# Kernel optimization log

Hardware: AMD Instinct MI355X
Metric: run time of the kernel (lower is better)

## Reference

```python
import jax, jax.numpy as jnp
import numpy as np

EPS = 1e-6
DIM_HEAD = 32
INP = 128
OUP = 128
IH = IW = 32


def _conv3x3(x, w):
    # NCHW conv, 3x3, stride 1, pad 1, no bias
    return jax.lax.conv_general_dilated(
        x, w, window_strides=(1, 1), padding=((1, 1), (1, 1)),
        dimension_numbers=("NCHW", "OIHW", "NCHW"))


def _groupnorm1(x, gamma, beta):
    # GroupNorm with 1 group: normalize over (C,H,W) per sample
    m = jnp.mean(x, axis=(1, 2, 3), keepdims=True)
    v = jnp.var(x, axis=(1, 2, 3), keepdims=True)
    xn = (x - m) * jax.lax.rsqrt(v + EPS)
    return xn * gamma[None, :, None, None] + beta[None, :, None, None]


def _proj(x, w, gamma, beta):
    return jax.nn.gelu(_groupnorm1(_conv3x3(x, w), gamma, beta), approximate=False)


def _relative_index(ih, iw):
    coords = np.stack(np.meshgrid(np.arange(ih), np.arange(iw), indexing="ij"))
    coords = coords.reshape(2, -1)  # (2, N)
    rel = coords[:, :, None] - coords[:, None, :]  # (2, N, N)
    rel[0] += ih - 1
    rel[1] += iw - 1
    rel[0] *= 2 * iw - 1
    return rel.sum(0).reshape(-1).astype(np.int32)  # (N*N,)


def setup_inputs() -> dict:
    key = jax.random.key(0)
    ks = jax.random.split(key, 12)
    B = 16
    x = jax.random.normal(ks[0], (B, INP, IH, IW), jnp.float32)
    w_scale = 0.05
    wq = jax.random.normal(ks[1], (INP, INP, 3, 3), jnp.float32) * w_scale
    wk = jax.random.normal(ks[2], (INP, INP, 3, 3), jnp.float32) * w_scale
    wv = jax.random.normal(ks[3], (INP, INP, 3, 3), jnp.float32) * w_scale
    gq = jnp.ones((INP,), jnp.float32); bq = jnp.zeros((INP,), jnp.float32)
    gk = jnp.ones((INP,), jnp.float32); bk = jnp.zeros((INP,), jnp.float32)
    gv = jnp.ones((INP,), jnp.float32); bv = jnp.zeros((INP,), jnp.float32)
    heads = INP // DIM_HEAD
    table = jax.random.normal(ks[4], ((2 * IH - 1) * (2 * IW - 1), heads), jnp.float32) * 0.02
    rel_index = jnp.asarray(_relative_index(IH, IW))
    out_w = jax.random.normal(ks[5], (OUP, INP, 1, 1), jnp.float32) * w_scale
    out_b = jnp.zeros((OUP,), jnp.float32)
    return {"x": x, "wq": wq, "gq": gq, "bq": bq, "wk": wk, "gk": gk, "bk": bk,
            "wv": wv, "gv": gv, "bv": bv, "table": table, "rel_index": rel_index,
            "out_w": out_w, "out_b": out_b}


def reference(x, wq, gq, bq, wk, gk, bk, wv, gv, bv, table, rel_index, out_w, out_b):
    B, C, ih, iw = x.shape
    H = C // DIM_HEAD
    N = ih * iw

    def to_heads(t):
        # b c ih iw -> b (ihiw) c -> b h n d (heads-major channel split)
        return t.reshape(B, C, N).transpose(0, 2, 1).reshape(B, N, H, DIM_HEAD).transpose(0, 2, 1, 3)

    q = to_heads(_proj(x, wq, gq, bq))
    k = to_heads(_proj(x, wk, gk, bk))
    v = to_heads(_proj(x, wv, gv, bv))

    # NOTE: original applies self.scale only when y is not None; y=None here -> no scale
    dots = jnp.einsum("bhnd,bhmd->bhnm", q, k)  # (B,H,N,N)

    bias = table[rel_index]                 # (N*N, H)
    bias = bias.reshape(N, N, H).transpose(2, 0, 1)[None]  # (1,H,N,N)
    attn = jax.nn.softmax(dots + bias, axis=-1)

    out = jnp.einsum("bhnm,bhmd->bhnd", attn, v)
    out = out.transpose(0, 2, 1, 3).reshape(B, N, C).transpose(0, 2, 1).reshape(B, C, ih, iw)
    # to_out: 1x1 conv + bias (Dropout2d is identity in eval)
    out = jax.lax.conv_general_dilated(
        out, out_w, window_strides=(1, 1), padding=((0, 0), (0, 0)),
        dimension_numbers=("NCHW", "OIHW", "NCHW")) + out_b[None, :, None, None]
    return out
```

## Files before the change

kernel.cpp:

```cpp
#include <hip/hip_runtime.h>

typedef unsigned short u16;
typedef unsigned int   u32;

#define NB   16
#define NC   128
#define NPIX 1024
#define NH   4
#define DH   32

typedef __attribute__((ext_vector_type(8))) short short8;
typedef __attribute__((ext_vector_type(4))) float f32x4;
typedef __attribute__((ext_vector_type(8))) _Float16 half8;

#define XROWS 1152

__device__ __forceinline__ float bf2f(u16 u) {
    return __uint_as_float(((u32)u) << 16);
}
__device__ __forceinline__ u16 f2bf(float f) {
    u32 u = __float_as_uint(f);
    u32 r = (u + 0x7fffu + ((u >> 16) & 1u)) >> 16;
    return (u16)r;
}
__device__ __forceinline__ u16 f2h(float f) {
    _Float16 h = (_Float16)f;
    u16 r; __builtin_memcpy(&r, &h, 2); return r;
}
__device__ __forceinline__ float h2f(u16 u) {
    _Float16 h; __builtin_memcpy(&h, &u, 2); return (float)h;
}
__device__ __forceinline__ int pk_h2(float a, float b) {
    auto h = __builtin_amdgcn_cvt_pkrtz(a, b);
    int r; __builtin_memcpy(&r, &h, 4); return r;
}
__device__ __forceinline__ float loadf(const void* p, int i, int isf) {
    return isf ? ((const float*)p)[i] : bf2f(((const u16*)p)[i]);
}
__device__ __forceinline__ float4 load4(const void* p, int i4, int isf) {
    if (isf) return ((const float4*)p)[i4];
    ushort4 u = ((const ushort4*)p)[i4];
    return make_float4(bf2f(u.x), bf2f(u.y), bf2f(u.z), bf2f(u.w));
}
__device__ __forceinline__ int detect_isf(const void* x) {
    const u16* p = (const u16*)x;
    u16 v = p[threadIdx.x & 63];
    int e = (v >> 7) & 0xFF;
    unsigned long long m = __ballot(e >= 134);
    return m != 0ull ? 1 : 0;
}

__global__ __launch_bounds__(256) void prep_all(
        const void* __restrict__ x,
        const void* __restrict__ w0, const void* __restrict__ w1,
        const void* __restrict__ w2, const void* __restrict__ ow,
        const int* __restrict__ rel, const void* __restrict__ table,
        u16* __restrict__ Wt, u16* __restrict__ Wf, u16* __restrict__ xTp,
        u16* __restrict__ biasT, float* __restrict__ stats) {
    __shared__ __align__(16) u32 smem_u[4160];
    int isf = detect_isf(x);
    int bid = blockIdx.x;
    int t = threadIdx.x;

    if (bid < 1792) {
        if (bid == 0 && t < 96) stats[t] = 0.f;
        int i = bid * 256 + t;
        if (i < 442368) {
            int j   = i / 147456;
            int rr  = i % 147456;
            int tap = rr >> 14;
            int co  = (rr >> 7) & 127;
            int ci  = rr & 127;
            const void* w = (j == 0) ? w0 : ((j == 1) ? w1 : w2);
            float v = loadf(w, (co * 128 + ci) * 9 + tap, isf);
            int coh = (co >> 6) & 1, wm = (co >> 5) & 1;
            int mt  = (co >> 4) & 1, l16 = co & 15;
            int ks  = (ci >> 5) & 3, q  = (ci >> 3) & 3, e = ci & 7;
            int dst = (j * 9 + tap) * 16384
                    + (coh * 2 + wm) * 4096 + ks * 1024 + mt * 512
                    + (q * 16 + l16) * 8 + e;
            Wt[dst] = f2bf(v);
        } else {
            int i2 = i - 442368;
            if (i2 < 16384) {
                int co = i2 >> 7, k = i2 & 127;
                int zc = (co >> 6) & 1, wm = (co >> 5) & 1;
                int mt = (co >> 4) & 1, l16 = co & 15;
                int ks = (k >> 5) & 3, q = (k >> 3) & 3, e = k & 7;
                int dst = (zc * 2 + wm) * 4096 + ks * 1024 + mt * 512
                        + (q * 16 + l16) * 8 + e;
                Wf[dst] = f2h(loadf(ow, i2, isf));
            }
        }
    } else if (bid < 2304) {
        float* tile = (float*)smem_u;
        int b2 = bid - 1792;
        int pixg = b2 & 7, cig = (b2 >> 3) & 3, b = b2 >> 5;

        if (pixg == 0 || pixg == 7) {
            int row = (pixg == 0 ? 0 : 1088) + (t >> 2);
            int seg = t & 3;
            size_t dst = ((size_t)(b * XROWS + row)) * 128 + cig * 32 + seg * 8;
            *(uint4*)&xTp[dst] = make_uint4(0, 0, 0, 0);
        }

        int ci = t >> 3, px0 = (t & 7) * 16;
        int base = b * (NC * NPIX) + (cig * 32 + ci) * NPIX + pixg * 128 + px0;
#pragma unroll
        for (int u = 0; u < 4; ++u) {
            float4 v = load4(x, (base >> 2) + u, isf);
            float* d = &tile[ci * 129 + px0 + u * 4];
            d[0] = v.x; d[1] = v.y; d[2] = v.z; d[3] = v.w;
        }
        __syncthreads();
#pragma unroll
        for (int u = 0; u < 2; ++u) {
            int c = t + u * 256;
            int pix = c >> 2, seg = c & 3;
            u16 tmp[8];
#pragma unroll
            for (int e = 0; e < 8; ++e)
                tmp[e] = f2bf(tile[(seg * 8 + e) * 129 + pix]);
            size_t dst = ((size_t)(b * XROWS + 64 + pixg * 128 + pix)) * 128
                       + cig * 32 + seg * 8;
            *(ushort4*)&xTp[dst] =
                make_ushort4(tmp[0], tmp[1], tmp[2], tmp[3]);
            *(ushort4*)&xTp[dst + 4] =
                make_ushort4(tmp[4], tmp[5], tmp[6], tmp[7]);
        }
    } else {
        int* rl = (int*)smem_u;
        int b2 = bid - 2304;
        int nt = b2 & 15, mt = b2 >> 4;

#pragma unroll
        for (int c = 0; c < 16; ++c) {
            int i = t + c * 256;
            int r = i >> 6, cc = i & 63;
            rl[r * 65 + cc] = rel[(size_t)(nt * 64 + r) * 1024 + mt * 64 + cc];
        }
        __syncthreads();

#pragma unroll
        for (int h = 0; h < NH; ++h) {
#pragma unroll
            for (int c = 0; c < 16; ++c) {
                int wdx = t + c * 256;
                int r     = wdx & 3;
                int lane  = (wdx >> 2) & 63;
                int fragl = wdx >> 8;
                int n16l  = fragl >> 2;
                int m16l  = fragl & 3;
                int n_loc = n16l * 16 + (lane & 15);
                int m_loc = m16l * 16 + ((lane >> 4) << 2) + r;
                int ri = rl[n_loc * 65 + m_loc];
                float v = loadf(table, ri * NH + h, isf);
                biasT[((size_t)h << 20)
                      + ((size_t)((nt * 4 + n16l) * 64 + (mt * 4 + m16l)) << 8)
                      + lane * 4 + r] = f2bf(v);
            }
        }
    }
}

__global__ __launch_bounds__(256) void conv6_kernel(
        const u16* __restrict__ xTp, const u16* __restrict__ Wt,
        u16* __restrict__ conv_out, float* __restrict__ stats) {
    __shared__ __align__(16) u16 Xh[194 * 128];

    int t = threadIdx.x;
    int bx = blockIdx.x, b = blockIdx.y, j = blockIdx.z;
    int pt = bx >> 1, coh = bx & 1;
    int p0 = pt * 128;
    int w = t >> 6, lane = t & 63;
    int q = lane >> 4, l16 = lane & 15;
    int cobase = coh * 64 + (w & 1) * 32;
    int pixbase = (w >> 1) * 64;

    const u16* xb  = xTp + ((size_t)b * XROWS + 64) * 128;
    const u16* wrb = Wt + (size_t)(j * 9) * 16384
                   + (coh * 2 + (w & 1)) * 4096 + lane * 8;

    short8 awA[2][4], awB[2][4];
#pragma unroll
    for (int ks = 0; ks < 4; ++ks) {
        awA[0][ks] = *(const short8*)(wrb + ks * 1024);
        awA[1][ks] = *(const short8*)(wrb + ks * 1024 + 512);
    }

#pragma unroll
    for (int k = 0; k < 13; ++k) {
        int c = t + k * 256;
        if (c < 194 * 16) {
            int row = c >> 4, seg = c & 15;
            int pg = p0 - 33 + row;
            uint4 v = *(const uint4*)(xb + (size_t)pg * 128 + seg * 8);
            *(uint4*)&Xh[row * 128 + ((seg + row) & 15) * 8] = v;
        }
    }
    __syncthreads();

    f32x4 acc[2][4];
#pragma unroll
    for (int mt = 0; mt < 2; ++mt)
#pragma unroll
        for (int nt = 0; nt < 4; ++nt) acc[mt][nt] = (f32x4)0.f;

#pragma unroll
    for (int tap = 0; tap < 9; ++tap) {
        const int dy = tap / 3, dx = tap % 3;
        bool inv_e = (dx == 0) && (l16 == 0);
        bool inv_o = (dx == 2) && (l16 == 15);
        int rbase = pixbase + dy * 32 + dx + l16;

        if (tap < 8) {
            const u16* nw = wrb + (size_t)(tap + 1) * 16384;
            if ((tap & 1) == 0) {
#pragma unroll
                for (int ks = 0; ks < 4; ++ks) {
                    awB[0][ks] = *(const short8*)(nw + ks * 1024);
                    awB[1][ks] = *(const short8*)(nw + ks * 1024 + 512);
                }
            } else {
#pragma unroll
                for (int ks = 0; ks < 4; ++ks) {
                    awA[0][ks] = *(const short8*)(nw + ks * 1024);
                    awA[1][ks] = *(const short8*)(nw + ks * 1024 + 512);
                }
            }
        }

#pragma unroll
        for (int ks = 0; ks < 4; ++ks) {
            int sl = ks * 4 + q;
            short8 bf[4];
#pragma unroll
            for (int nt = 0; nt < 4; ++nt) {
                int row = rbase + nt * 16;
                short8 v = *(const short8*)&Xh[row * 128
                                               + ((sl + row) & 15) * 8];
                bf[nt] = ((nt & 1) ? inv_o : inv_e) ? (short8)0 : v;
            }
#pragma unroll
            for (int mt = 0; mt < 2; ++mt) {
                short8 a = ((tap & 1) == 0) ? awA[mt][ks] : awB[mt][ks];
#pragma unroll
                for (int nt = 0; nt < 4; ++nt)
                    acc[mt][nt] = __builtin_amdgcn_mfma_f32_16x16x32_bf16(
                        a, bf[nt], acc[mt][nt], 0, 0, 0);
            }
        }
    }

    float s = 0.f, s2 = 0.f;
    int z = j * NB + b;
    int co16b  = coh * 4 + (w & 1) * 2;
    int pix16b = pt * 8 + (w >> 1) * 4;
#pragma unroll
    for (int mt = 0; mt < 2; ++mt) {
#pragma unroll
        for (int nt = 0; nt < 4; ++nt) {
            f32x4 v = acc[mt][nt];
            u16 ev[4];
#pragma unroll
            for (int r = 0; r < 4; ++r) {
                float val = v[r];
                ev[r] = f2h(val);
                s += val;
                s2 = fmaf(val, val, s2);
            }
            uint2 pw;
            __builtin_memcpy(&pw, ev, 8);
            size_t addr = (size_t)z * 131072
                        + (size_t)(co16b + mt) * 16384
                        + (size_t)(pix16b + nt) * 256 + lane * 4;
            *(uint2*)&conv_out[addr] = pw;
        }
    }
#pragma unroll
    for (int off = 32; off; off >>= 1) {
        s  += __shfl_down(s,  (unsigned)off, 64);
        s2 += __shfl_down(s2, (unsigned)off, 64);
    }
    if (lane == 0) {
        atomicAdd(&stats[(j * NB + b) * 2 + 0], s);
        atomicAdd(&stats[(j * NB + b) * 2 + 1], s2);
    }
}

__global__ __launch_bounds__(256) void norm_kernel(
        const void* __restrict__ xdet,
        const u16* __restrict__ convF, const float* __restrict__ stats,
        const void* __restrict__ g0, const void* __restrict__ b0,
        const void* __restrict__ g1, const void* __restrict__ b1,
        const void* __restrict__ g2, const void* __restrict__ b2,
        u16* __restrict__ qh, u16* __restrict__ kh, u16* __restrict__ vh) {
    int isf = detect_isf(xdet);
    int t = threadIdx.x;
    int x = blockIdx.x;
    int h = blockIdx.y;
    int z = blockIdx.z;
    int j = z >> 4;
    int b = z & 15;
    const void* gam = (j == 0) ? g0 : ((j == 1) ? g1 : g2);
    const void* bet = (j == 0) ? b0 : ((j == 1) ? b1 : b2);

    float sum = stats[z * 2], ss = stats[z * 2 + 1];
    const float inv = 1.0f / 131072.0f;
    float mean = sum * inv;
    float var  = fmaxf(ss * inv - mean * mean, 0.f);
    float rstd = rsqrtf(var + 1e-6f);

    int lane = t & 63, fi = t >> 6;
    int q2 = lane >> 4, l16 = lane & 15;

    const size_t zbase = (size_t)z * 131072;
    u16* qkdst = ((j == 0) ? qh : kh) + ((size_t)(b * NH + h)) * NPIX * DH;
    u16* vdst  = vh + ((size_t)(b * NH + h)) * DH * NPIX;

#pragma unroll
    for (int p = 0; p < 8; ++p) {
        int fgi   = p * 4 + fi;
        int co16l = fgi >> 4;
        int pix16l = fgi & 15;
        int co16  = h * 2 + co16l;
        int pix16 = x * 16 + pix16l;
        const u16* src = convF + zbase + (size_t)co16 * 16384
                       + (size_t)pix16 * 256 + lane * 4;
        uint2 wv = *(const uint2*)src;
        u16 ev[4];
        __builtin_memcpy(ev, &wv, 8);

        int cl0 = co16l * 16 + q2 * 4;
        int pix = pix16 * 16 + l16;

        float o[4];
#pragma unroll
        for (int r = 0; r < 4; ++r) {
            float v = h2f(ev[r]);
            v = (v - mean) * rstd * loadf(gam, h * DH + cl0 + r, isf)
              + loadf(bet, h * DH + cl0 + r, isf);
            o[r] = 0.5f * v * (1.0f + erff(v * 0.70710678118654752f));
        }

        if (j == 2) {
#pragma unroll
            for (int r = 0; r < 4; ++r)
                vdst[(size_t)(cl0 + r) * NPIX + pix] = f2h(o[r]);
        } else {
            uint2 pw = make_uint2((u32)pk_h2(o[0], o[1]),
                                  (u32)pk_h2(o[2], o[3]));
            *(uint2*)(qkdst + (size_t)pix * DH + cl0) = pw;
        }
    }
}

__global__ __launch_bounds__(256) void attn2_kernel(
        const u16* __restrict__ qh, const u16* __restrict__ kh,
        const u16* __restrict__ vh, const u16* __restrict__ biasT,
        u16* __restrict__ attfh) {
    __shared__ __align__(16) u16 Kl[2][128 * 40];
    __shared__ __align__(16) u16 Vl[2][32 * 136];

    int t = threadIdx.x;
    int f = blockIdx.x;
    int r_ = f >> 3;
    int g = (f & 7) * 4 + (r_ >> 4);
    int b = r_ & 15;
    int h = g & 3, qt = g >> 2;
    int w = t >> 6, lane = t & 63, q = lane >> 4, l16 = lane & 15;
    int nrow0 = qt * 128 + w * 32;

    const u16* qb = qh + (((size_t)(b * NH + h)) * NPIX) * DH;
    const u16* kb = kh + (((size_t)(b * NH + h)) * NPIX) * DH;
    const u16* vb = vh + (((size_t)(b * NH + h)) * DH) * NPIX;
    const u16* bf0 = biasT + ((size_t)h << 20)
                   + ((size_t)(qt * 8 + w * 2 + 0) << 14) + lane * 4;
    const u16* bf1 = biasT + ((size_t)h << 20)
                   + ((size_t)(qt * 8 + w * 2 + 1) << 14) + lane * 4;

    int krow = t >> 2, kseg = t & 3;
    int vrow = t >> 4, vseg = t & 15;

    {
        uint4 k0 = *(const uint4*)(kb + t * 8);
        uint4 k1 = *(const uint4*)(kb + (t + 256) * 8);
        uint4 v0 = *(const uint4*)(vb + vrow * NPIX + vseg * 8);
        uint4 v1 = *(const uint4*)(vb + (vrow + 16) * NPIX + vseg * 8);
        *(uint4*)&Kl[0][krow * 40 + kseg * 8] = k0;
        *(uint4*)&Kl[0][(krow + 64) * 40 + kseg * 8] = k1;
        *(uint4*)&Vl[0][vrow * 136 + vseg * 8] = v0;
        *(uint4*)&Vl[0][(vrow + 16) * 136 + vseg * 8] = v1;
    }

    half8 qf[2];
#pragma unroll
    for (int nt = 0; nt < 2; ++nt)
        qf[nt] = *(const half8*)(qb + (size_t)(nrow0 + nt * 16 + l16) * DH
                                 + q * 8);

    f32x4 O[2][2];
#pragma unroll
    for (int dt = 0; dt < 2; ++dt)
#pragma unroll
        for (int nt = 0; nt < 2; ++nt) O[dt][nt] = (f32x4)0.f;
    float mrow[2] = {-1e30f, -1e30f}, lrow[2] = {0.f, 0.f};

    __syncthreads();

    for (int kc = 0; kc < 8; ++kc) {
        int cur = kc & 1;
        const u16* Kc = &Kl[cur][0];
        const u16* Vc = &Vl[cur][0];

        uint4 pk0, pk1, pv0, pv1;
        bool pf = (kc < 7);
        if (pf) {
            int m0n = (kc + 1) * 128;
            pk0 = *(const uint4*)(kb + m0n * 32 + t * 8);
            pk1 = *(const uint4*)(kb + m0n * 32 + (t + 256) * 8);
            pv0 = *(const uint4*)(vb + vrow * NPIX + m0n + vseg * 8);
            pv1 = *(const uint4*)(vb + (vrow + 16) * NPIX + m0n + vseg * 8);
        }

        f32x4 St[8][2];
#pragma unroll
        for (int mt = 0; mt < 8; ++mt) {
            half8 kf = *(const half8*)&Kc[(mt * 16 + l16) * 40 + q * 8];
            int m16 = kc * 8 + mt;
            ushort4 bv0 = *(const ushort4*)(bf0 + (m16 << 8));
            ushort4 bv1 = *(const ushort4*)(bf1 + (m16 << 8));
            f32x4 c0, c1;
            c0[0] = bf2f(bv0.x); c0[1] = bf2f(bv0.y);
            c0[2] = bf2f(bv0.z); c0[3] = bf2f(bv0.w);
            c1[0] = bf2f(bv1.x); c1[1] = bf2f(bv1.y);
            c1[2] = bf2f(bv1.z); c1[3] = bf2f(bv1.w);
            St[mt][0] = __builtin_amdgcn_mfma_f32_16x16x32_f16(
                kf, qf[0], c0, 0, 0, 0);
            St[mt][1] = __builtin_amdgcn_mfma_f32_16x16x32_f16(
                kf, qf[1], c1, 0, 0, 0);
        }
        float mx[2] = {-1e30f, -1e30f};
#pragma unroll
        for (int mt = 0; mt < 8; ++mt)
#pragma unroll
            for (int nt = 0; nt < 2; ++nt)
#pragma unroll
                for (int r = 0; r < 4; ++r)
                    mx[nt] = fmaxf(mx[nt], St[mt][nt][r]);
        float alpha[2];
#pragma unroll
        for (int nt = 0; nt < 2; ++nt) {
            mx[nt] = fmaxf(mx[nt], __shfl_xor(mx[nt], 16, 64));
            mx[nt] = fmaxf(mx[nt], __shfl_xor(mx[nt], 32, 64));
            float mn = fmaxf(mrow[nt], mx[nt]);
            alpha[nt] = __expf(mrow[nt] - mn);
            mrow[nt] = mn;
        }
        float sm[2] = {0.f, 0.f};
#pragma unroll
        for (int mt = 0; mt < 8; ++mt)
#pragma unroll
            for (int nt = 0; nt < 2; ++nt)
#pragma unroll
                for (int r = 0; r < 4; ++r) {
                    float p = __expf(St[mt][nt][r] - mrow[nt]);
                    St[mt][nt][r] = p;
                    sm[nt] += p;
                }
#pragma unroll
        for (int nt = 0; nt < 2; ++nt) {
            sm[nt] += __shfl_xor(sm[nt], 16, 64);
            sm[nt] += __shfl_xor(sm[nt], 32, 64);
            lrow[nt] = lrow[nt] * alpha[nt] + sm[nt];
        }
        if (!__all(alpha[0] == 1.0f && alpha[1] == 1.0f)) {
#pragma unroll
            for (int dt = 0; dt < 2; ++dt)
#pragma unroll
                for (int nt = 0; nt < 2; ++nt)
#pragma unroll
                    for (int r = 0; r < 4; ++r)
                        O[dt][nt][r] *= alpha[nt];
        }
#pragma unroll
        for (int ms = 0; ms < 4; ++ms) {
            half8 vf[2];
#pragma unroll
            for (int dt = 0; dt < 2; ++dt) {
                const u16* vrow_p = &Vc[(dt * 16 + l16) * 136 + ms * 32];
                uint2 lo = *(const uint2*)(vrow_p + q * 4);
                uint2 hi = *(const uint2*)(vrow_p + 16 + q * 4);
                uint4 cmb = make_uint4(lo.x, lo.y, hi.x, hi.y);
                __builtin_memcpy(&vf[dt], &cmb, 16);
            }
#pragma unroll
            for (int nt = 0; nt < 2; ++nt) {
                int pw[4];
                pw[0] = pk_h2(St[2 * ms][nt][0],     St[2 * ms][nt][1]);
                pw[1] = pk_h2(St[2 * ms][nt][2],     St[2 * ms][nt][3]);
                pw[2] = pk_h2(St[2 * ms + 1][nt][0], St[2 * ms + 1][nt][1]);
                pw[3] = pk_h2(St[2 * ms + 1][nt][2], St[2 * ms + 1][nt][3]);
                half8 pf2; __builtin_memcpy(&pf2, pw, 16);
#pragma unroll
                for (int dt = 0; dt < 2; ++dt)
                    O[dt][nt] = __builtin_amdgcn_mfma_f32_16x16x32_f16(
                        vf[dt], pf2, O[dt][nt], 0, 0, 0);
            }
        }
        if (pf) {
            *(uint4*)&Kl[cur ^ 1][krow * 40 + kseg * 8] = pk0;
            *(uint4*)&Kl[cur ^ 1][(krow + 64) * 40 + kseg * 8] = pk1;
            *(uint4*)&Vl[cur ^ 1][vrow * 136 + vseg * 8] = pv0;
            *(uint4*)&Vl[cur ^ 1][(vrow + 16) * 136 + vseg * 8] = pv1;
        }
        __syncthreads();
    }

#pragma unroll
    for (int nt = 0; nt < 2; ++nt) {
        float rl = 1.0f / lrow[nt];
        int n = nrow0 + nt * 16 + l16;
        u16* dst = attfh + ((size_t)b * NPIX + n) * NC + h * DH;
#pragma unroll
        for (int dt = 0; dt < 2; ++dt) {
            f32x4 o = O[dt][nt];
            uint2 pv = make_uint2((u32)pk_h2(o[0] * rl, o[1] * rl),
                                  (u32)pk_h2(o[2] * rl, o[3] * rl));
            *(uint2*)(dst + dt * 16 + q * 4) = pv;
        }
    }
}

__global__ __launch_bounds__(256) void out3_kernel(
        const void* __restrict__ xdet,
        const u16* __restrict__ attfh, const u16* __restrict__ Wf,
        const void* __restrict__ ob, void* __restrict__ out) {
    int isf = detect_isf(xdet);
    int t = threadIdx.x;
    int n0 = blockIdx.x * 64, b = blockIdx.y, zc = blockIdx.z;
    int w = t >> 6, lane = t & 63, q = lane >> 4, l16 = lane & 15;
    int cobase = zc * 64 + (w & 1) * 32, nbase = (w >> 1) * 32;

    f32x4 acc[2][2];
#pragma unroll
    for (int mt = 0; mt < 2; ++mt)
#pragma unroll
        for (int nt = 0; nt < 2; ++nt) acc[mt][nt] = (f32x4)0.f;

    const u16* ab = attfh + ((size_t)b * NPIX + n0 + nbase) * NC;
    const u16* wfb = Wf + (zc * 2 + (w & 1)) * 4096 + lane * 8;
#pragma unroll
    for (int ks = 0; ks < 4; ++ks) {
        int k0 = ks * 32 + q * 8;
        half8 a[2], bfr[2];
#pragma unroll
        for (int mt = 0; mt < 2; ++mt)
            a[mt] = *(const half8*)(wfb + ks * 1024 + mt * 512);
#pragma unroll
        for (int nt = 0; nt < 2; ++nt)
            bfr[nt] = *(const half8*)(ab + (size_t)(nt * 16 + l16) * NC + k0);
#pragma unroll
        for (int mt = 0; mt < 2; ++mt)
#pragma unroll
            for (int nt = 0; nt < 2; ++nt)
                acc[mt][nt] = __builtin_amdgcn_mfma_f32_16x16x32_f16(
                    a[mt], bfr[nt], acc[mt][nt], 0, 0, 0);
    }

#pragma unroll
    for (int mt = 0; mt < 2; ++mt) {
#pragma unroll
        for (int nt = 0; nt < 2; ++nt) {
            f32x4 v = acc[mt][nt];
            int n = n0 + nbase + nt * 16 + l16;
#pragma unroll
            for (int r = 0; r < 4; ++r) {
                int co = cobase + mt * 16 + q * 4 + r;
                float val = v[r] + loadf(ob, co, isf);
                size_t oidx = ((size_t)b * NC + co) * NPIX + n;
                if (isf) ((float*)out)[oidx] = val;
                else     ((u16*)out)[oidx]   = f2bf(val);
            }
        }
    }
}

extern "C" void kernel_launch(void* const* d_in, const int* in_sizes, int n_in,
                              void* d_out, int out_size, void* d_ws,
                              size_t ws_size, hipStream_t stream) {
    (void)in_sizes; (void)n_in; (void)out_size; (void)ws_size;
    const void* x     = d_in[0];
    const void* wq    = d_in[1];
    const void* gq    = d_in[2];
    const void* bq    = d_in[3];
    const void* wk    = d_in[4];
    const void* gk    = d_in[5];
    const void* bk    = d_in[6];
    const void* wv    = d_in[7];
    const void* gv    = d_in[8];
    const void* bv    = d_in[9];
    const void* table = d_in[10];
    const int*  rel   = (const int*)d_in[11];
    const void* ow    = d_in[12];
    const void* ob    = d_in[13];

    char* ws = (char*)d_ws;
    float* stats = (float*)(ws);
    char*  regQ  = ws + 512;
    u16*   xTp   = (u16*)regQ;
    u16*   Wt    = (u16*)(regQ + 5242880);
    u16*   qhp   = (u16*)regQ;
    u16*   khp   = (u16*)(regQ + 4194304);
    u16*   vhp   = (u16*)(regQ + 8388608);
    u16*   biasT = (u16*)(regQ + 12582912);
    u16*   Wf    = (u16*)(regQ + 20971520);
    char*  regA  = regQ + 25165824;
    u16*   conv  = (u16*)regA;
    u16*   attfh = (u16*)(regA + 16777216);

    prep_all<<<2560, 256, 0, stream>>>(x, wq, wk, wv, ow, rel, table,
                                       Wt, Wf, xTp, biasT, stats);
    conv6_kernel<<<dim3(16, 16, 3), 256, 0, stream>>>(xTp, Wt, conv, stats);
    norm_kernel<<<dim3(4, 4, 48), 256, 0, stream>>>(x, conv, stats,
                                                    gq, bq, gk, bk, gv, bv,
                                                    qhp, khp, vhp);
    attn2_kernel<<<512, 256, 0, stream>>>(qhp, khp, vhp, biasT, attfh);
    out3_kernel<<<dim3(16, 16, 2), 256, 0, stream>>>(x, attfh, Wf, ob, d_out);
}
```

Before: 189.0 us.

## Store attention output in MFMA fragment layout and vectorize bias-table gather

The attention kernel now writes its output directly in the fragment-packed layout that the output projection's MFMA B operand expects, using one 16-byte store per lane instead of two 8-byte scattered stores. The out3 kernel reads these fragments with contiguous per-lane loads. The output weight prepack permutes the k index to match the new intra-fragment element order. Separately, the bias-table preprocessing gathers all four heads with a single float4 load per index instead of four scalar loads. The cost is a tighter coupling of the intermediate layout and the weight permutation across kernels.

```diff
diff --git a/kernel.cpp b/kernel.cpp
--- a/kernel.cpp
+++ b/kernel.cpp
@@ -86,9 +86,12 @@
                 int co = i2 >> 7, k = i2 & 127;
                 int zc = (co >> 6) & 1, wm = (co >> 5) & 1;
                 int mt = (co >> 4) & 1, l16 = co & 15;
-                int ks = (k >> 5) & 3, q = (k >> 3) & 3, e = k & 7;
+                int ks = k >> 5, c = k & 31;
+                int qf, ef;
+                if (c < 16) { qf = c >> 2;        ef = c & 3; }
+                else        { qf = (c - 16) >> 2; ef = 4 + ((c - 16) & 3); }
                 int dst = (zc * 2 + wm) * 4096 + ks * 1024 + mt * 512
-                        + (q * 16 + l16) * 8 + e;
+                        + (qf * 16 + l16) * 8 + ef;
                 Wf[dst] = f2h(loadf(ow, i2, isf));
             }
         }
@@ -142,23 +145,23 @@
         __syncthreads();
 
 #pragma unroll
-        for (int h = 0; h < NH; ++h) {
-#pragma unroll
-            for (int c = 0; c < 16; ++c) {
-                int wdx = t + c * 256;
-                int r     = wdx & 3;
-                int lane  = (wdx >> 2) & 63;
-                int fragl = wdx >> 8;
-                int n16l  = fragl >> 2;
-                int m16l  = fragl & 3;
-                int n_loc = n16l * 16 + (lane & 15);
-                int m_loc = m16l * 16 + ((lane >> 4) << 2) + r;
-                int ri = rl[n_loc * 65 + m_loc];
-                float v = loadf(table, ri * NH + h, isf);
-                biasT[((size_t)h << 20)
-                      + ((size_t)((nt * 4 + n16l) * 64 + (mt * 4 + m16l)) << 8)
-                      + lane * 4 + r] = f2bf(v);
-            }
+        for (int c = 0; c < 16; ++c) {
+            int wdx = t + c * 256;
+            int r     = wdx & 3;
+            int lane  = (wdx >> 2) & 63;
+            int fragl = wdx >> 8;
+            int n16l  = fragl >> 2;
+            int m16l  = fragl & 3;
+            int n_loc = n16l * 16 + (lane & 15);
+            int m_loc = m16l * 16 + ((lane >> 4) << 2) + r;
+            int ri = rl[n_loc * 65 + m_loc];
+            float4 tv = load4(table, ri, isf);
+            float tvh[4] = {tv.x, tv.y, tv.z, tv.w};
+            size_t off = ((size_t)((nt * 4 + n16l) * 64 + (mt * 4 + m16l))
+                          << 8) + lane * 4 + r;
+#pragma unroll
+            for (int h = 0; h < NH; ++h)
+                biasT[((size_t)h << 20) + off] = f2bf(tvh[h]);
         }
     }
 }
@@ -174,7 +177,6 @@
     int p0 = pt * 128;
     int w = t >> 6, lane = t & 63;
     int q = lane >> 4, l16 = lane & 15;
-    int cobase = coh * 64 + (w & 1) * 32;
     int pixbase = (w >> 1) * 64;
 
     const u16* xb  = xTp + ((size_t)b * XROWS + 64) * 128;
@@ -517,30 +519,30 @@
         __syncthreads();
     }
 
+    int pix16b = nrow0 >> 4;
 #pragma unroll
     for (int nt = 0; nt < 2; ++nt) {
         float rl = 1.0f / lrow[nt];
-        int n = nrow0 + nt * 16 + l16;
-        u16* dst = attfh + ((size_t)b * NPIX + n) * NC + h * DH;
-#pragma unroll
-        for (int dt = 0; dt < 2; ++dt) {
-            f32x4 o = O[dt][nt];
-            uint2 pv = make_uint2((u32)pk_h2(o[0] * rl, o[1] * rl),
-                                  (u32)pk_h2(o[2] * rl, o[3] * rl));
-            *(uint2*)(dst + dt * 16 + q * 4) = pv;
-        }
+        f32x4 o0 = O[0][nt], o1 = O[1][nt];
+        uint4 pw = make_uint4((u32)pk_h2(o0[0] * rl, o0[1] * rl),
+                              (u32)pk_h2(o0[2] * rl, o0[3] * rl),
+                              (u32)pk_h2(o1[0] * rl, o1[1] * rl),
+                              (u32)pk_h2(o1[2] * rl, o1[3] * rl));
+        *(uint4*)&attfh[(((size_t)(b * 64 + pix16b + nt) * 4 + h) << 9)
+                        + lane * 8] = pw;
     }
 }
 
 __global__ __launch_bounds__(256) void out3_kernel(
         const void* __restrict__ xdet,
-        const u16* __restrict__ attfh, const u16* __restrict__ Wf,
+        const u16* __restrict__ attfB, const u16* __restrict__ Wf,
         const void* __restrict__ ob, void* __restrict__ out) {
     int isf = detect_isf(xdet);
     int t = threadIdx.x;
     int n0 = blockIdx.x * 64, b = blockIdx.y, zc = blockIdx.z;
     int w = t >> 6, lane = t & 63, q = lane >> 4, l16 = lane & 15;
     int cobase = zc * 64 + (w & 1) * 32, nbase = (w >> 1) * 32;
+    int p16b = (n0 + nbase) >> 4;
 
     f32x4 acc[2][2];
 #pragma unroll
@@ -548,18 +550,17 @@
 #pragma unroll
         for (int nt = 0; nt < 2; ++nt) acc[mt][nt] = (f32x4)0.f;
 
-    const u16* ab = attfh + ((size_t)b * NPIX + n0 + nbase) * NC;
     const u16* wfb = Wf + (zc * 2 + (w & 1)) * 4096 + lane * 8;
 #pragma unroll
     for (int ks = 0; ks < 4; ++ks) {
-        int k0 = ks * 32 + q * 8;
         half8 a[2], bfr[2];
 #pragma unroll
         for (int mt = 0; mt < 2; ++mt)
             a[mt] = *(const half8*)(wfb + ks * 1024 + mt * 512);
 #pragma unroll
         for (int nt = 0; nt < 2; ++nt)
-            bfr[nt] = *(const half8*)(ab + (size_t)(nt * 16 + l16) * NC + k0);
+            bfr[nt] = *(const half8*)&attfB[
+                (((size_t)(b * 64 + p16b + nt) * 4 + ks) << 9) + lane * 8];
 #pragma unroll
         for (int mt = 0; mt < 2; ++mt)
 #pragma unroll
```

Measured after the change: 183.5 us. -2.9%, faster.
